# Optimization experiments

Measured on AMD Instinct MI355X. Metric: run time of the kernel, lower is better.

The kernel has to match this reference:

```python
import jax, jax.numpy as jnp
import numpy as np

STATE_DIM, ACTION_DIM, HIDDEN_DIM = 512, 64, 2048
INPUT_DIM = STATE_DIM + ACTION_DIM + 1  # 577
BATCH = 4096


def setup_inputs() -> dict:
    key = jax.random.key(0)
    ks = jax.random.split(key, 12)
    sc_x = 1.0 / np.sqrt(INPUT_DIM)
    sc_h = 1.0 / np.sqrt(HIDDEN_DIM)
    return {
        "s": jax.random.normal(ks[0], (BATCH, STATE_DIM), jnp.float32),
        "a_prev": jax.random.normal(ks[1], (BATCH, ACTION_DIM), jnp.float32),
        "r_prev": jax.random.normal(ks[2], (BATCH, 1), jnp.float32),
        "h": jnp.zeros((HIDDEN_DIM,), jnp.float32),
        "c": jnp.zeros((HIDDEN_DIM,), jnp.float32),
        # Fused gate weights: columns ordered [i, f, g(c-tilde), o]
        "Wx": jax.random.uniform(ks[3], (INPUT_DIM, 4 * HIDDEN_DIM), jnp.float32, -sc_x, sc_x),
        "Wh": jax.random.uniform(ks[4], (HIDDEN_DIM, 4 * HIDDEN_DIM), jnp.float32, -sc_h, sc_h),
        "bh": jax.random.uniform(ks[5], (4 * HIDDEN_DIM,), jnp.float32, -sc_h, sc_h),
        "Wa": jax.random.uniform(ks[6], (HIDDEN_DIM, ACTION_DIM), jnp.float32, -sc_h, sc_h),
        "ba": jax.random.uniform(ks[7], (ACTION_DIM,), jnp.float32, -sc_h, sc_h),
        "Wv": jax.random.uniform(ks[8], (HIDDEN_DIM, 1), jnp.float32, -sc_h, sc_h),
        "bv": jax.random.uniform(ks[9], (1,), jnp.float32, -sc_h, sc_h),
    }


def reference(s, a_prev, r_prev, h, c, Wx, Wh, bh, Wa, ba, Wv, bv):
    # x: [B, input_dim]
    x = jnp.concatenate([s, a_prev, r_prev], axis=1)
    # Two fused GEMMs replace the 8 separate small linears (same math).
    z = x @ Wx + h @ Wh + bh          # [B, 4H]
    zi, zf, zg, zo = jnp.split(z, 4, axis=-1)
    i = jax.nn.sigmoid(zi)
    f = jax.nn.sigmoid(zf)
    c_new = f * c + i * jnp.tanh(zg)  # [B, H] (c broadcast over batch)
    o = jax.nn.sigmoid(zo)
    h_new = o * jnp.tanh(c_new)       # [B, H]
    probs = jax.nn.softmax(h_new @ Wa + ba, axis=1)  # [B, A]
    v = h_new @ Wv + bv               # [B, 1]
    return (probs, v)
```

## Files before the change

kernel.cpp:

```cpp
#include <hip/hip_runtime.h>
#include <hip/hip_bf16.h>

#define BATCH   4096
#define SDIM    512
#define ADIM    64
#define IDIM    577
#define KP2     576
#define NKT64   9
#define HDIM    2048
#define ZDIM    8192
#define BUFE    (128 * 64)

typedef __attribute__((ext_vector_type(8))) __bf16 bf16x8;
typedef __attribute__((ext_vector_type(4))) float  accx4;

__global__ __launch_bounds__(256) void setup_kernel(
    const float* __restrict__ s, const float* __restrict__ a_prev,
    const float* __restrict__ h,
    const float* __restrict__ wx, const float* __restrict__ wh,
    const float* __restrict__ wa,
    __hip_bfloat16* __restrict__ xb, __hip_bfloat16* __restrict__ wxt,
    __hip_bfloat16* __restrict__ waT, float* __restrict__ zh_w)
{
    __shared__ float stile[64 * 65];
    const int bid = blockIdx.x;
    const int t = threadIdx.x;

    if (bid < 1152) {
        const int kt2 = bid >> 7;
        const int nt  = bid & 127;
        const int c4  = t & 15;
        const int rr  = t >> 4;
#pragma unroll
        for (int i = 0; i < 4; ++i) {
            const int r = rr + i * 16;
            const int k = kt2 * 64 + r;
            float4 v =
                *(const float4*)(wx + (size_t)k * ZDIM + nt * 64 + c4 * 4);
            *(float4*)(stile + r * 65 + c4 * 4) = v;
        }
        __syncthreads();
        const int ch = t & 7;
#pragma unroll
        for (int i = 0; i < 2; ++i) {
            const int nr = (t >> 3) + i * 32;
            bf16x8 w8;
#pragma unroll
            for (int j = 0; j < 8; ++j)
                w8[j] = (__bf16)stile[(ch * 8 + j) * 65 + nr];
            *(bf16x8*)(wxt + (size_t)(nt * 64 + nr) * KP2 + kt2 * 64 + ch * 8)
                = w8;
        }
    } else if (bid < 1664) {
        const int zb = bid - 1152;
        const int nb = zb & 31, ky = zb >> 5;
        const int n  = nb * 256 + t;
        const float* hp  = h + ky * 128;
        const float* whp = wh + (size_t)ky * 128 * ZDIM + n;
        float p = 0.0f;
#pragma unroll 32
        for (int kk = 0; kk < 128; ++kk)
            p = fmaf(hp[kk], whp[(size_t)kk * ZDIM], p);
        zh_w[ky * ZDIM + n] = p;
    } else if (bid < 5760) {
        const int row = bid - 1664;
        const float* srow = s + (size_t)row * SDIM;
        const float* arow = a_prev + (size_t)row * ADIM;
        __hip_bfloat16* xrow = xb + (size_t)row * KP2;
        for (int c = t; c < KP2; c += 256) {
            const float v = (c < SDIM) ? srow[c] : arow[c - SDIM];
            xrow[c] = __float2bfloat16(v);
        }
    } else {
        const int wb = bid - 5760;
        const int kt = wb >> 1, at = wb & 1;
        const int c  = t & 31, r0 = t >> 5;
#pragma unroll
        for (int i = 0; i < 4; ++i) {
            int r = r0 + i * 8;
            stile[r * 33 + c] = wa[(size_t)(kt * 32 + r) * ADIM + at * 32 + c];
        }
        __syncthreads();
#pragma unroll
        for (int i = 0; i < 4; ++i) {
            int r = r0 + i * 8;
            waT[(size_t)(at * 32 + r) * HDIM + kt * 32 + c] =
                __float2bfloat16(stile[c * 33 + r]);
        }
    }
}

__device__ __forceinline__ float rcp_f(float x) {
    return __builtin_amdgcn_rcpf(x);
}
__device__ __forceinline__ float sigmoid_f(float x) {
    return rcp_f(1.0f + __expf(-x));
}
__device__ __forceinline__ float tanh_f(float x) {
    return 1.0f - 2.0f * rcp_f(1.0f + __expf(2.0f * x));
}

__global__ __launch_bounds__(256, 2) void lstm_gemm(
    const __hip_bfloat16* __restrict__ xb,
    const __hip_bfloat16* __restrict__ wxt,
    const float* __restrict__ zh_w,
    const float* __restrict__ bh,
    const float* __restrict__ cvec,
    const float* __restrict__ wx,
    const float* __restrict__ r_prev,
    __hip_bfloat16* __restrict__ hout)
{
    __shared__ __bf16 smA[2 * BUFE];
    __shared__ __bf16 smB[2 * BUFE];
    const int t    = threadIdx.x;
    const int lane = t & 63;
    const int wid  = t >> 6;
    const int m0   = blockIdx.x * 128;
    const int n0   = blockIdx.y * 32;
    const int wm   = wid >> 1, wn = wid & 1;
    const int fl15 = lane & 15;
    const int fhi  = lane >> 4;

    accx4 acc[4][4] = {};

    const int srow = lane >> 3;
    const int slot = lane & 7;
    const int cch  = slot ^ srow;
    const __bf16* gA[4]; const __bf16* gB[4]; int lofs[4];
#pragma unroll
    for (int i = 0; i < 4; ++i) {
        const int r = wid * 32 + i * 8 + srow;
        gA[i] = (const __bf16*)xb + (size_t)(m0 + r) * KP2 + cch * 8;
        const int g = r >> 5, nn = r & 31;
        gB[i] = (const __bf16*)wxt +
                (size_t)(g * HDIM + n0 + nn) * KP2 + cch * 8;
        lofs[i] = (wid * 32 + i * 8) * 64;
    }

    auto stage = [&](int tile, int p) {
        const int ko = tile * 64;
        const int po = p * BUFE;
#pragma unroll
        for (int i = 0; i < 4; ++i) {
            __builtin_amdgcn_global_load_lds(
                (const __attribute__((address_space(1))) void*)(gA[i] + ko),
                (__attribute__((address_space(3))) void*)(smA + po + lofs[i]),
                16, 0, 0);
            __builtin_amdgcn_global_load_lds(
                (const __attribute__((address_space(1))) void*)(gB[i] + ko),
                (__attribute__((address_space(3))) void*)(smB + po + lofs[i]),
                16, 0, 0);
        }
    };

    auto compute = [&](int p) {
        const int po = p * BUFE;
#pragma unroll
        for (int hf = 0; hf < 2; ++hf) {
            const int ck = hf * 4 + fhi;
            const int sl = (ck ^ (fl15 & 7)) * 8;
            bf16x8 af[4], bfr[4];
#pragma unroll
            for (int rt = 0; rt < 4; ++rt)
                af[rt] = *(const bf16x8*)(smA + po +
                    (wm * 64 + rt * 16 + fl15) * 64 + sl);
#pragma unroll
            for (int g = 0; g < 4; ++g)
                bfr[g] = *(const bf16x8*)(smB + po +
                    (g * 32 + wn * 16 + fl15) * 64 + sl);
#pragma unroll
            for (int g = 0; g < 4; ++g)
#pragma unroll
                for (int rt = 0; rt < 4; ++rt)
                    acc[g][rt] = __builtin_amdgcn_mfma_f32_16x16x32_bf16(
                        af[rt], bfr[g], acc[g][rt], 0, 0, 0);
        }
    };

    stage(0, 0);
    __syncthreads();
#pragma unroll
    for (int kt = 0; kt < NKT64 - 1; ++kt) {
        stage(kt + 1, (kt + 1) & 1);
        compute(kt & 1);
        __syncthreads();
    }
    compute((NKT64 - 1) & 1);

    const int colg = n0 + wn * 16 + fl15;
    float zsum[4], wxr[4];
#pragma unroll
    for (int g = 0; g < 4; ++g) {
        float z = bh[g * HDIM + colg];
#pragma unroll
        for (int j = 0; j < 16; ++j)
            z += zh_w[j * ZDIM + g * HDIM + colg];
        zsum[g] = z;
        wxr[g] = wx[(size_t)576 * ZDIM + g * HDIM + colg];
    }
    const float cv = cvec[colg];
#pragma unroll
    for (int rt = 0; rt < 4; ++rt) {
#pragma unroll
        for (int r = 0; r < 4; ++r) {
            const int row = m0 + wm * 64 + rt * 16 + (fhi << 2) + r;
            const float rv = r_prev[row];
            const float zi = acc[0][rt][r] + zsum[0] + rv * wxr[0];
            const float zf = acc[1][rt][r] + zsum[1] + rv * wxr[1];
            const float zg = acc[2][rt][r] + zsum[2] + rv * wxr[2];
            const float zo = acc[3][rt][r] + zsum[3] + rv * wxr[3];
            const float cn = sigmoid_f(zf) * cv + sigmoid_f(zi) * tanh_f(zg);
            const float hn = sigmoid_f(zo) * tanh_f(cn);
            hout[(size_t)row * HDIM + colg] = __float2bfloat16(hn);
        }
    }
}

__global__ __launch_bounds__(512) void head_kernel(
    const __hip_bfloat16* __restrict__ hnew,
    const __hip_bfloat16* __restrict__ waT,
    const float* __restrict__ wv,
    const float* __restrict__ ba, const float* __restrict__ bv,
    float* __restrict__ probs, float* __restrict__ vout)
{
    __shared__ float lg[8][16][68];
    __shared__ float vpart[8][16];
    const int t    = threadIdx.x;
    const int lane = t & 63;
    const int w    = t >> 6;
    const int r0   = blockIdx.x * 16;
    const int fl15 = lane & 15, fhi = lane >> 4;
    const int k0   = w * 256;

    const __bf16* arow = (const __bf16*)hnew +
        (size_t)(r0 + fl15) * HDIM + k0 + fhi * 8;
    const __bf16* brow = (const __bf16*)waT +
        (size_t)fl15 * HDIM + k0 + fhi * 8;
    const float* wvp = wv + k0 + fhi * 8;

    accx4 acc[4] = {};
    float va0 = 0.f, va1 = 0.f;
#pragma unroll
    for (int kk = 0; kk < 256; kk += 32) {
        bf16x8 af = *(const bf16x8*)(arow + kk);
#pragma unroll
        for (int a = 0; a < 4; ++a) {
            bf16x8 bf = *(const bf16x8*)(brow + (size_t)a * 16 * HDIM + kk);
            acc[a] = __builtin_amdgcn_mfma_f32_16x16x32_bf16(
                af, bf, acc[a], 0, 0, 0);
        }
#pragma unroll
        for (int j = 0; j < 4; ++j) {
            va0 = fmaf((float)af[j],     wvp[kk + j],     va0);
            va1 = fmaf((float)af[j + 4], wvp[kk + j + 4], va1);
        }
    }
#pragma unroll
    for (int a = 0; a < 4; ++a)
#pragma unroll
        for (int r = 0; r < 4; ++r)
            lg[w][fhi * 4 + r][a * 16 + fl15] = acc[a][r];
    float va = va0 + va1;
    va += __shfl_xor(va, 16);
    va += __shfl_xor(va, 32);
    if (lane < 16) vpart[w][lane] = va;
    __syncthreads();

    const float bav = ba[lane];
#pragma unroll
    for (int i = 0; i < 2; ++i) {
        const int row = w * 2 + i;
        float logit = bav;
#pragma unroll
        for (int p = 0; p < 8; ++p)
            logit += lg[p][row][lane];
        float m = logit;
#pragma unroll
        for (int mask = 32; mask >= 1; mask >>= 1)
            m = fmaxf(m, __shfl_xor(m, mask));
        const float e = __expf(logit - m);
        float ssum = e;
#pragma unroll
        for (int mask = 32; mask >= 1; mask >>= 1)
            ssum += __shfl_xor(ssum, mask);
        probs[(size_t)(r0 + row) * 64 + lane] = e / ssum;
    }
    if (t < 16) {
        float v = bv[0];
#pragma unroll
        for (int p = 0; p < 8; ++p)
            v += vpart[p][t];
        vout[r0 + t] = v;
    }
}

extern "C" void kernel_launch(void* const* d_in, const int* in_sizes, int n_in,
                              void* d_out, int out_size, void* d_ws,
                              size_t ws_size, hipStream_t stream)
{
    const float* s      = (const float*)d_in[0];
    const float* a_prev = (const float*)d_in[1];
    const float* r_prev = (const float*)d_in[2];
    const float* h      = (const float*)d_in[3];
    const float* c      = (const float*)d_in[4];
    const float* Wx     = (const float*)d_in[5];
    const float* Wh     = (const float*)d_in[6];
    const float* bh     = (const float*)d_in[7];
    const float* Wa     = (const float*)d_in[8];
    const float* ba     = (const float*)d_in[9];
    const float* Wv     = (const float*)d_in[10];
    const float* bv     = (const float*)d_in[11];

    float* out   = (float*)d_out;
    float* probs = out;
    float* vout  = out + (size_t)BATCH * ADIM;

    char* ws = (char*)d_ws;
    __hip_bfloat16* xb   = (__hip_bfloat16*)ws;
    __hip_bfloat16* wxt  = (__hip_bfloat16*)(ws + 4718592);
    __hip_bfloat16* waT  = (__hip_bfloat16*)(ws + 14155776);
    float* zh_w          = (float*)(ws + 14417920);
    __hip_bfloat16* hnew = (__hip_bfloat16*)(ws + 14942208);

    setup_kernel<<<5888, 256, 0, stream>>>(
        s, a_prev, h, Wx, Wh, Wa, xb, wxt, waT, zh_w);
    lstm_gemm<<<dim3(BATCH / 128, HDIM / 32), 256, 0, stream>>>(
        xb, wxt, zh_w, bh, c, Wx, r_prev, hnew);
    head_kernel<<<BATCH / 16, 512, 0, stream>>>(
        hnew, waT, Wv, ba, bv, probs, vout);
}
```

Measured before the change: 205.3 us.

## Halve K-tile to 32 for four blocks per CU with single-barrier pipeline

Shrinks the staged K tile from 64 to 32, halving LDS per block so the GEMM kernel can target four blocks per CU instead of two. The swizzle pattern and the global-to-LDS load mapping are redone for 32-wide rows. The main loop now issues the next stage after one explicit waitcnt and barrier per iteration instead of two syncs. This trades twice as many barriers and shorter MFMA bursts per tile for higher occupancy, and the tighter register budget may cause spills.

```diff
diff --git a/kernel.cpp b/kernel.cpp
--- a/kernel.cpp
+++ b/kernel.cpp
@@ -6,10 +6,10 @@
 #define ADIM    64
 #define IDIM    577
 #define KP2     576
-#define NKT64   9
+#define NKT32   18
 #define HDIM    2048
 #define ZDIM    8192
-#define BUFE    (128 * 64)
+#define BUFE    (128 * 32)
 
 typedef __attribute__((ext_vector_type(8))) __bf16 bf16x8;
 typedef __attribute__((ext_vector_type(4))) float  accx4;
@@ -100,7 +100,7 @@
     return 1.0f - 2.0f * rcp_f(1.0f + __expf(2.0f * x));
 }
 
-__global__ __launch_bounds__(256, 2) void lstm_gemm(
+__global__ __launch_bounds__(256, 4) void lstm_gemm(
     const __hip_bfloat16* __restrict__ xb,
     const __hip_bfloat16* __restrict__ wxt,
     const float* __restrict__ zh_w,
@@ -123,25 +123,24 @@
 
     accx4 acc[4][4] = {};
 
-    const int srow = lane >> 3;
-    const int slot = lane & 7;
-    const int cch  = slot ^ srow;
-    const __bf16* gA[4]; const __bf16* gB[4]; int lofs[4];
-#pragma unroll
-    for (int i = 0; i < 4; ++i) {
-        const int r = wid * 32 + i * 8 + srow;
-        gA[i] = (const __bf16*)xb + (size_t)(m0 + r) * KP2 + cch * 8;
-        const int g = r >> 5, nn = r & 31;
+    const int lrow = lane >> 2;
+    const int lsl  = lane & 3;
+    const int cch  = lsl ^ ((lane >> 3) & 3);
+    const __bf16* gA[2]; const __bf16* gB[2]; int lofs[2];
+#pragma unroll
+    for (int i = 0; i < 2; ++i) {
+        const int rA = wid * 32 + i * 16 + lrow;
+        gA[i] = (const __bf16*)xb + (size_t)(m0 + rA) * KP2 + cch * 8;
         gB[i] = (const __bf16*)wxt +
-                (size_t)(g * HDIM + n0 + nn) * KP2 + cch * 8;
-        lofs[i] = (wid * 32 + i * 8) * 64;
+                (size_t)(wid * HDIM + n0 + i * 16 + lrow) * KP2 + cch * 8;
+        lofs[i] = (wid * 32 + i * 16) * 32;
     }
 
     auto stage = [&](int tile, int p) {
-        const int ko = tile * 64;
+        const int ko = tile * 32;
         const int po = p * BUFE;
 #pragma unroll
-        for (int i = 0; i < 4; ++i) {
+        for (int i = 0; i < 2; ++i) {
             __builtin_amdgcn_global_load_lds(
                 (const __attribute__((address_space(1))) void*)(gA[i] + ko),
                 (__attribute__((address_space(3))) void*)(smA + po + lofs[i]),
@@ -153,39 +152,35 @@
         }
     };
 
+    const int slr = (fhi ^ ((fl15 >> 1) & 3)) * 8;
+
     auto compute = [&](int p) {
         const int po = p * BUFE;
-#pragma unroll
-        for (int hf = 0; hf < 2; ++hf) {
-            const int ck = hf * 4 + fhi;
-            const int sl = (ck ^ (fl15 & 7)) * 8;
-            bf16x8 af[4], bfr[4];
+        bf16x8 af[4], bfr[4];
+#pragma unroll
+        for (int rt = 0; rt < 4; ++rt)
+            af[rt] = *(const bf16x8*)(smA + po +
+                (wm * 64 + rt * 16 + fl15) * 32 + slr);
+#pragma unroll
+        for (int g = 0; g < 4; ++g)
+            bfr[g] = *(const bf16x8*)(smB + po +
+                (g * 32 + wn * 16 + fl15) * 32 + slr);
+#pragma unroll
+        for (int g = 0; g < 4; ++g)
 #pragma unroll
             for (int rt = 0; rt < 4; ++rt)
-                af[rt] = *(const bf16x8*)(smA + po +
-                    (wm * 64 + rt * 16 + fl15) * 64 + sl);
-#pragma unroll
-            for (int g = 0; g < 4; ++g)
-                bfr[g] = *(const bf16x8*)(smB + po +
-                    (g * 32 + wn * 16 + fl15) * 64 + sl);
-#pragma unroll
-            for (int g = 0; g < 4; ++g)
-#pragma unroll
-                for (int rt = 0; rt < 4; ++rt)
-                    acc[g][rt] = __builtin_amdgcn_mfma_f32_16x16x32_bf16(
-                        af[rt], bfr[g], acc[g][rt], 0, 0, 0);
-        }
+                acc[g][rt] = __builtin_amdgcn_mfma_f32_16x16x32_bf16(
+                    af[rt], bfr[g], acc[g][rt], 0, 0, 0);
     };
 
     stage(0, 0);
-    __syncthreads();
-#pragma unroll
-    for (int kt = 0; kt < NKT64 - 1; ++kt) {
-        stage(kt + 1, (kt + 1) & 1);
+#pragma unroll
+    for (int kt = 0; kt < NKT32; ++kt) {
+        asm volatile("s_waitcnt vmcnt(0)" ::: "memory");
+        asm volatile("s_barrier" ::: "memory");
+        if (kt + 1 < NKT32) stage(kt + 1, (kt + 1) & 1);
         compute(kt & 1);
-        __syncthreads();
-    }
-    compute((NKT64 - 1) & 1);
+    }
 
     const int colg = n0 + wn * 16 + fl15;
     float zsum[4], wxr[4];
```

Measured after the change: 228.1 us. 11.1% more time.

## Preswizzle x into MFMA fragment layout and load A fragments straight to registers

Applied to the files above, without the earlier changes.

The setup kernel now writes bf16 x in the fragment-tiled order the 16x16x32 MFMA expects. The GEMM can then load its A operand directly from global memory into registers, register-double-buffered, instead of staging it through LDS. Only the B weights still go through LDS, now in three buffers with a single barrier per k-tile and hand-written vmcnt waits. Occupancy is raised to 3 blocks per CU. This removes the LDS traffic and LDS footprint for A and overlaps more loads, at the cost of higher register pressure and fragile manual wait counts.

```diff
diff --git a/kernel.cpp b/kernel.cpp
--- a/kernel.cpp
+++ b/kernel.cpp
@@ -9,7 +9,7 @@
 #define NKT64   9
 #define HDIM    2048
 #define ZDIM    8192
-#define BUFE    (128 * 64)
+#define BUFB    (128 * 64)
 
 typedef __attribute__((ext_vector_type(8))) __bf16 bf16x8;
 typedef __attribute__((ext_vector_type(4))) float  accx4;
@@ -64,12 +64,25 @@
         zh_w[ky * ZDIM + n] = p;
     } else if (bid < 5760) {
         const int row = bid - 1664;
-        const float* srow = s + (size_t)row * SDIM;
-        const float* arow = a_prev + (size_t)row * ADIM;
-        __hip_bfloat16* xrow = xb + (size_t)row * KP2;
-        for (int c = t; c < KP2; c += 256) {
-            const float v = (c < SDIM) ? srow[c] : arow[c - SDIM];
-            xrow[c] = __float2bfloat16(v);
+        if (t < 72) {
+            const int ch  = t;
+            const int t16 = row >> 4, fl = row & 15;
+            float4 v0, v1;
+            if (ch < 64) {
+                v0 = *(const float4*)(s + (size_t)row * SDIM + ch * 8);
+                v1 = *(const float4*)(s + (size_t)row * SDIM + ch * 8 + 4);
+            } else {
+                v0 = *(const float4*)(a_prev + (size_t)row * ADIM + (ch - 64) * 8);
+                v1 = *(const float4*)(a_prev + (size_t)row * ADIM + (ch - 64) * 8 + 4);
+            }
+            bf16x8 w;
+            w[0] = (__bf16)v0.x; w[1] = (__bf16)v0.y;
+            w[2] = (__bf16)v0.z; w[3] = (__bf16)v0.w;
+            w[4] = (__bf16)v1.x; w[5] = (__bf16)v1.y;
+            w[6] = (__bf16)v1.z; w[7] = (__bf16)v1.w;
+            const int kc32 = ch >> 2, sub = ch & 3;
+            *(bf16x8*)((__bf16*)xb +
+                ((size_t)(t16 * 18 + kc32) * 64 + sub * 16 + fl) * 8) = w;
         }
     } else {
         const int wb = bid - 5760;
@@ -100,8 +113,8 @@
     return 1.0f - 2.0f * rcp_f(1.0f + __expf(2.0f * x));
 }
 
-__global__ __launch_bounds__(256, 2) void lstm_gemm(
-    const __hip_bfloat16* __restrict__ xb,
+__global__ __launch_bounds__(256, 3) void lstm_gemm(
+    const __hip_bfloat16* __restrict__ xbf,
     const __hip_bfloat16* __restrict__ wxt,
     const float* __restrict__ zh_w,
     const float* __restrict__ bh,
@@ -110,12 +123,12 @@
     const float* __restrict__ r_prev,
     __hip_bfloat16* __restrict__ hout)
 {
-    __shared__ __bf16 smA[2 * BUFE];
-    __shared__ __bf16 smB[2 * BUFE];
+    __shared__ __bf16 smB[3 * BUFB];
     const int t    = threadIdx.x;
     const int lane = t & 63;
     const int wid  = t >> 6;
     const int m0   = blockIdx.x * 128;
+    const int m16  = blockIdx.x * 8;
     const int n0   = blockIdx.y * 32;
     const int wm   = wid >> 1, wn = wid & 1;
     const int fl15 = lane & 15;
@@ -126,44 +139,44 @@
     const int srow = lane >> 3;
     const int slot = lane & 7;
     const int cch  = slot ^ srow;
-    const __bf16* gA[4]; const __bf16* gB[4]; int lofs[4];
+    const __bf16* gB[4]; int lofs[4];
 #pragma unroll
     for (int i = 0; i < 4; ++i) {
         const int r = wid * 32 + i * 8 + srow;
-        gA[i] = (const __bf16*)xb + (size_t)(m0 + r) * KP2 + cch * 8;
         const int g = r >> 5, nn = r & 31;
         gB[i] = (const __bf16*)wxt +
                 (size_t)(g * HDIM + n0 + nn) * KP2 + cch * 8;
         lofs[i] = (wid * 32 + i * 8) * 64;
     }
 
-    auto stage = [&](int tile, int p) {
+    auto stageB = [&](int tile, int buf) {
         const int ko = tile * 64;
-        const int po = p * BUFE;
-#pragma unroll
-        for (int i = 0; i < 4; ++i) {
-            __builtin_amdgcn_global_load_lds(
-                (const __attribute__((address_space(1))) void*)(gA[i] + ko),
-                (__attribute__((address_space(3))) void*)(smA + po + lofs[i]),
-                16, 0, 0);
+        const int po = buf * BUFB;
+#pragma unroll
+        for (int i = 0; i < 4; ++i)
             __builtin_amdgcn_global_load_lds(
                 (const __attribute__((address_space(1))) void*)(gB[i] + ko),
                 (__attribute__((address_space(3))) void*)(smB + po + lofs[i]),
                 16, 0, 0);
-        }
     };
 
-    auto compute = [&](int p) {
-        const int po = p * BUFE;
+    const __bf16* abase = (const __bf16*)xbf + lane * 8;
+    auto loadA = [&](int tile, bf16x8 (&dst)[8]) {
+#pragma unroll
+        for (int rt = 0; rt < 4; ++rt)
+#pragma unroll
+            for (int hf = 0; hf < 2; ++hf)
+                dst[rt * 2 + hf] = *(const bf16x8*)(abase +
+                    (size_t)((m16 + wm * 4 + rt) * 18 + tile * 2 + hf) * 512);
+    };
+
+    auto compute = [&](int buf, const bf16x8 (&aR)[8]) {
+        const int po = buf * BUFB;
 #pragma unroll
         for (int hf = 0; hf < 2; ++hf) {
             const int ck = hf * 4 + fhi;
             const int sl = (ck ^ (fl15 & 7)) * 8;
-            bf16x8 af[4], bfr[4];
-#pragma unroll
-            for (int rt = 0; rt < 4; ++rt)
-                af[rt] = *(const bf16x8*)(smA + po +
-                    (wm * 64 + rt * 16 + fl15) * 64 + sl);
+            bf16x8 bfr[4];
 #pragma unroll
             for (int g = 0; g < 4; ++g)
                 bfr[g] = *(const bf16x8*)(smB + po +
@@ -173,19 +186,28 @@
 #pragma unroll
                 for (int rt = 0; rt < 4; ++rt)
                     acc[g][rt] = __builtin_amdgcn_mfma_f32_16x16x32_bf16(
-                        af[rt], bfr[g], acc[g][rt], 0, 0, 0);
+                        aR[rt * 2 + hf], bfr[g], acc[g][rt], 0, 0, 0);
         }
     };
 
-    stage(0, 0);
-    __syncthreads();
-#pragma unroll
-    for (int kt = 0; kt < NKT64 - 1; ++kt) {
-        stage(kt + 1, (kt + 1) & 1);
-        compute(kt & 1);
-        __syncthreads();
-    }
-    compute((NKT64 - 1) & 1);
+    bf16x8 aA[8], aB[8];
+
+    stageB(0, 0);
+    loadA(0, aA);
+    stageB(1, 1);
+#pragma unroll
+    for (int kt = 0; kt < NKT64; ++kt) {
+        if (kt < NKT64 - 1)
+            asm volatile("s_waitcnt vmcnt(4)" ::: "memory");
+        else
+            asm volatile("s_waitcnt vmcnt(0)" ::: "memory");
+        asm volatile("s_barrier" ::: "memory");
+        if (kt + 1 < NKT64) {
+            if (kt & 1) loadA(kt + 1, aA); else loadA(kt + 1, aB);
+        }
+        if (kt + 2 < NKT64) stageB(kt + 2, (kt + 2) % 3);
+        if (kt & 1) compute(kt % 3, aB); else compute(kt % 3, aA);
+    }
 
     const int colg = n0 + wn * 16 + fl15;
     float zsum[4], wxr[4];
```

New measurement: 227.5 us. 1.11x slower.
